# Optimization experiments

Measured on AMD Instinct MI355X. Metric: run time of the kernel, lower is better.

Reference implementation:

```python
import jax, jax.numpy as jnp
import numpy as np

N, E, DIN, D, FE, L, B, M = 10000, 40000, 11, 64, 4, 4, 512, 3


def setup_inputs() -> dict:
    key = jax.random.key(0)
    ks = iter(jax.random.split(key, 24))
    s = lambda *sh: jax.random.normal(next(ks), sh, jnp.float32)
    return {
        "x": s(N, DIN),
        "edge_index": jax.random.randint(next(ks), (2, E), 0, N),
        "edge_attr": jax.random.uniform(next(ks), (E, FE), jnp.float32),
        "batch": jnp.sort(jax.random.randint(next(ks), (N,), 0, B)),
        "W0": s(DIN, D) * 0.1, "b0": jnp.zeros((D,), jnp.float32),
        "Wn1": s(FE, 2 * D) * 0.1, "bn1": jnp.zeros((2 * D,), jnp.float32),
        "Wn2": s(2 * D, D * D) * 0.02, "bn2": jnp.zeros((D * D,), jnp.float32),
        "root": s(L, D, D) * 0.1, "conv_bias": jnp.zeros((L, D), jnp.float32),
        "lstm_Wih": s(4 * D, 2 * D) * 0.1, "lstm_Whh": s(4 * D, D) * 0.1,
        "lstm_b": jnp.zeros((4 * D,), jnp.float32),
        "Wo1": s(2 * D, D) * 0.1, "bo1": jnp.zeros((D,), jnp.float32),
        "Wo2": s(D, 1) * 0.1, "bo2": jnp.zeros((1,), jnp.float32),
    }


def reference(x, edge_index, edge_attr, batch, W0, b0, Wn1, bn1, Wn2, bn2,
              root, conv_bias, lstm_Wih, lstm_Whh, lstm_b, Wo1, bo1, Wo2, bo2):
    src, dst = edge_index[0], edge_index[1]
    h = x @ W0 + b0  # [N, D]
    # Edge MLP is SHARED across all conv layers -> compute per-edge weight matrices once
    ew = (jax.nn.silu(edge_attr @ Wn1 + bn1) @ Wn2 + bn2).reshape(E, D, D)
    for l in range(L):
        msg = jnp.einsum('ed,edf->ef', h[src], ew)  # gather-compute per edge
        aggr = jax.ops.segment_sum(msg, dst, num_segments=N)  # scatter-add to targets
        h = h + (aggr + h @ root[l] + conv_bias[l])  # NNConv + residual
    # Set2Set pooling (LSTM, M processing steps)
    q_star = jnp.zeros((B, 2 * D), h.dtype)
    hs = jnp.zeros((B, D), h.dtype)
    cs = jnp.zeros((B, D), h.dtype)
    for _ in range(M):
        gates = q_star @ lstm_Wih.T + hs @ lstm_Whh.T + lstm_b
        i, f, g, o = jnp.split(gates, 4, axis=-1)  # torch LSTM gate order
        cs = jax.nn.sigmoid(f) * cs + jax.nn.sigmoid(i) * jnp.tanh(g)
        hs = jax.nn.sigmoid(o) * jnp.tanh(cs)
        q = hs  # [B, D]
        e = jnp.sum(h * q[batch], axis=-1)  # [N]
        emax = jax.ops.segment_max(e, batch, num_segments=B)
        ex = jnp.exp(e - emax[batch])
        denom = jax.ops.segment_sum(ex, batch, num_segments=B)
        a = ex / denom[batch]  # per-graph softmax attention
        r = jax.ops.segment_sum(a[:, None] * h, batch, num_segments=B)
        q_star = jnp.concatenate([q, r], axis=-1)
    out = jax.nn.silu(q_star @ Wo1 + bo1) @ Wo2 + bo2
    return out.reshape(-1)
```

## Files before the change

### kernel.cpp

```cpp
#include <hip/hip_runtime.h>
#include <cstdint>
#include <cstddef>

#define NN   10000
#define EE   40000
#define DIN_ 11
#define DD   64
#define LL   4
#define BB   512
#define MM   3
#define K1   128
#define DD2  4096
#define NPB  16
#define CSPL 2
#define CPB  4
#define ESLOT 12
#define ECREG (8 * ESLOT)
#define GSTR 512

typedef unsigned short ushort_t;
typedef unsigned int   uint_t;

typedef __bf16 bf16x8_t __attribute__((ext_vector_type(8)));
typedef float  f32x4_t  __attribute__((ext_vector_type(4)));
union FragU { uint4 u; bf16x8_t b; };

__device__ __forceinline__ float bfu(ushort_t u) { return __uint_as_float(((uint_t)u) << 16); }
__device__ __forceinline__ float bflo(uint_t u) { return __uint_as_float(u << 16); }
__device__ __forceinline__ float bfhi(uint_t u) { return __uint_as_float(u & 0xffff0000u); }
__device__ __forceinline__ ushort_t f2bf(float f) {
  uint_t u = __float_as_uint(f);
  u = (u + 0x7fffu + ((u >> 16) & 1u)) >> 16;
  return (ushort_t)u;
}
__device__ __forceinline__ uint_t pack2(float lo, float hi) {
  return (uint_t)f2bf(lo) | ((uint_t)f2bf(hi) << 16);
}
__device__ __forceinline__ float sigmf_(float x) { return 1.f / (1.f + expf(-x)); }
__device__ __forceinline__ float siluf_(float x) { return x / (1.f + expf(-x)); }

#if defined(__HIP_DEVICE_COMPILE__) && __has_builtin(__builtin_amdgcn_fdot2_f32_bf16)
typedef __bf16 bf16x2_t __attribute__((ext_vector_type(2)));
__device__ __forceinline__ float dot2a(uint_t a, uint_t b, float c) {
  union { uint_t u; bf16x2_t v; } ua, ub;
  ua.u = a; ub.u = b;
  return __builtin_amdgcn_fdot2_f32_bf16(ua.v, ub.v, c, false);
}
#else
__device__ __forceinline__ float dot2a(uint_t a, uint_t b, float c) {
  return c + bflo(a) * bflo(b) + bfhi(a) * bfhi(b);
}
#endif

__device__ __forceinline__ int detect_bf16(const void* ea) {
  const int lane = threadIdx.x & 63;
  uint_t v = ((const uint_t*)ea)[lane];
  ushort_t a = (ushort_t)(v & 0xffffu), b = (ushort_t)(v >> 16);
  bool bad = (a & 0x8000u) || a > 0x3F80u || (b & 0x8000u) || b > 0x3F80u;
  return __ballot(bad) == 0ull ? 1 : 0;
}
__device__ __forceinline__ float ldf(const void* p, size_t i, int isbf) {
  return isbf ? bfu(((const ushort_t*)p)[i]) : ((const float*)p)[i];
}

#define PB_EMB0 256
#define PB_HIST0 (PB_EMB0 + NN / 4)
#define PB_CAN0 (PB_HIST0 + (EE + 255) / 256)
#define PB_TOTAL (PB_CAN0 + 81)
__global__ __launch_bounds__(256) void k_prep(
    const void* __restrict__ ea, const void* __restrict__ Wn2, uint_t* __restrict__ wn2m,
    const void* __restrict__ Wih, const void* __restrict__ Whh,
    float* __restrict__ Wiht, float* __restrict__ Whht,
    const void* __restrict__ x, const void* __restrict__ W0, const void* __restrict__ b0,
    const void* __restrict__ bn2, float* __restrict__ h, uint_t* __restrict__ hpk,
    float* __restrict__ nbias,
    const int* __restrict__ ei, int* __restrict__ cnt_s,
    const void* __restrict__ root, const void* __restrict__ cb,
    float* __restrict__ rootc, float* __restrict__ bn2c, float* __restrict__ cbc) {
  __shared__ ushort_t row[DD2];
  __shared__ float xs4[4][DIN_];
  __shared__ float hl4[4][DD];
  const int bx = blockIdx.x, tid = threadIdx.x;
  const int isbf = detect_bf16(ea);

  if (bx < 128) {
    const int k = bx;
    if (isbf) {
      const uint4* src = (const uint4*)((const ushort_t*)Wn2 + (size_t)k * DD2);
      ((uint4*)row)[tid] = src[tid];
      ((uint4*)row)[tid + 256] = src[tid + 256];
    } else {
      const float* src = (const float*)Wn2 + (size_t)k * DD2;
      for (int j = 0; j < 16; ++j) row[tid + 256 * j] = f2bf(src[tid + 256 * j]);
    }
    __syncthreads();
    const int kpg = k >> 1, par = k & 1;
    const int lane = tid >> 2, jp = tid & 3;
    const int q = lane >> 4, n = lane & 15;
    for (int fc = 0; fc < 4; ++fc) {
#pragma unroll
      for (int hf = 0; hf < 2; ++hf) {
        int d0 = hf * 32 + q * 8 + 2 * jp;
        int f = fc * 16 + n;
        uint_t lo = row[d0 * 64 + f], hi = row[(d0 + 1) * 64 + f];
        wn2m[((((size_t)kpg * 4 + fc) * 2 + par) * 2 + hf) * 256 + tid] = lo | (hi << 16);
      }
    }
  } else if (bx < PB_EMB0) {
    int idx = (bx - 128) * 256 + tid;
    {
      int j = idx >> 7, i = idx & 127;
      Wiht[i * 256 + j] = ldf(Wih, idx, isbf);
    }
    if (idx < 4 * DD * DD) {
      int j = idx >> 6, i = idx & 63;
      Whht[i * 256 + j] = ldf(Whh, idx, isbf);
    }
  } else if (bx < PB_HIST0) {
    const int w = tid >> 6, f = tid & 63;
    const int n = (bx - PB_EMB0) * 4 + w;
    if (f < DIN_) xs4[w][f] = ldf(x, (size_t)n * DIN_ + f, isbf);
    __syncthreads();
    float a = ldf(b0, f, isbf);
    for (int i = 0; i < DIN_; ++i) a += xs4[w][i] * ldf(W0, i * DD + f, isbf);
    h[(size_t)n * DD + f] = a;
    hl4[w][f] = a;
    float other = __shfl_down(a, 1);
    if ((f & 1) == 0)
      hpk[(size_t)n * 32 + (f >> 1)] = pack2(a, other);
    __syncthreads();
    float nb = 0.f;
#pragma unroll
    for (int d = 0; d < DD; ++d) nb += hl4[w][d] * ldf(bn2, d * DD + f, isbf);
    nbias[(size_t)n * DD + f] = nb;
  } else if (bx < PB_CAN0) {
    int e = (bx - PB_HIST0) * 256 + tid;
    if (e < EE) atomicAdd(&cnt_s[ei[e]], 1);
  } else {
    int idx = (bx - PB_CAN0) * 256 + tid;
    if (idx < LL * DD2) rootc[idx] = ldf(root, idx, isbf);
    else if (idx < LL * DD2 + DD2) bn2c[idx - LL * DD2] = ldf(bn2, idx - LL * DD2, isbf);
    else if (idx < LL * DD2 + DD2 + LL * DD)
      cbc[idx - LL * DD2 - DD2] = ldf(cb, idx - LL * DD2 - DD2, isbf);
  }
}

__global__ void k_scan(const int* __restrict__ cnt, int* __restrict__ rp,
                       const int* __restrict__ batch, int* __restrict__ goff) {
  if (blockIdx.x == 1) {
    int g = threadIdx.x;
    if (g > BB) return;
    int lo = 0, hi = NN;
    while (lo < hi) {
      int mid = (lo + hi) >> 1;
      if (batch[mid] < g) lo = mid + 1; else hi = mid;
    }
    goff[g] = lo;
    return;
  }
  __shared__ int part[1024];
  const int tid = threadIdx.x;
  const int chunk = (NN + 1023) / 1024;
  int s = 0;
  for (int j = 0; j < chunk; ++j) {
    int idx = tid * chunk + j;
    if (idx < NN) s += cnt[idx];
  }
  part[tid] = s;
  __syncthreads();
  for (int off = 1; off < 1024; off <<= 1) {
    int v = (tid >= off) ? part[tid - off] : 0;
    __syncthreads();
    part[tid] += v;
    __syncthreads();
  }
  int base = (tid == 0) ? 0 : part[tid - 1];
  for (int j = 0; j < chunk; ++j) {
    int idx = tid * chunk + j;
    if (idx < NN) { rp[idx] = base; base += cnt[idx]; }
  }
  if (tid == 1023) rp[NN] = part[1023];
}

__global__ void k_fill(const int* __restrict__ ei, const int* __restrict__ rps,
                       int* __restrict__ cur_s, int* __restrict__ epos,
                       int* __restrict__ esd) {
  int e = blockIdx.x * 256 + threadIdx.x;
  if (e >= EE) return;
  int s = ei[e], d = ei[EE + e];
  int ps = atomicAdd(&cur_s[s], 1);
  int pos = rps[s] + ps;
  epos[e] = pos;
  esd[2 * pos] = s;
  esd[2 * pos + 1] = d;
}

__global__ void k_edgemlp(const void* __restrict__ ea, const void* __restrict__ Wn1,
                          const void* __restrict__ bn1, const int* __restrict__ epos,
                          uint_t* __restrict__ hn1c) {
  const int isbf = detect_bf16(ea);
  int idx = blockIdx.x * 256 + threadIdx.x;
  if (idx >= EE * (K1 / 2)) return;
  int e = idx >> 6, j = idx & 63;
  int k0 = 2 * j, k1 = 2 * j + 1;
  float a0 = ldf(ea, e * 4 + 0, isbf), a1 = ldf(ea, e * 4 + 1, isbf);
  float a2 = ldf(ea, e * 4 + 2, isbf), a3 = ldf(ea, e * 4 + 3, isbf);
  float t0 = ldf(bn1, k0, isbf) + a0 * ldf(Wn1, k0, isbf) + a1 * ldf(Wn1, K1 + k0, isbf)
           + a2 * ldf(Wn1, 2 * K1 + k0, isbf) + a3 * ldf(Wn1, 3 * K1 + k0, isbf);
  float t1 = ldf(bn1, k1, isbf) + a0 * ldf(Wn1, k1, isbf) + a1 * ldf(Wn1, K1 + k1, isbf)
           + a2 * ldf(Wn1, 2 * K1 + k1, isbf) + a3 * ldf(Wn1, 3 * K1 + k1, isbf);
  int pos = epos[e];
  hn1c[((size_t)(j >> 3) * EE + pos) * 8 + (j & 7)] = pack2(siluf_(t0), siluf_(t1));
}

__global__ __launch_bounds__(512, 4) void k_conv(
    const uint_t* __restrict__ hpk, const uint_t* __restrict__ hn1c,
    const uint_t* __restrict__ Wn2m, const float* __restrict__ nbias,
    const int* __restrict__ rps, const int* __restrict__ esd,
    float* __restrict__ aggr) {
  __shared__ uint_t Gp[NPB * GSTR];
  __shared__ int2 eStage[ECREG];
  const int tid = threadIdx.x;
  const int w = tid >> 6, lane = tid & 63;
  const int q = lane >> 4, n16 = lane & 15;
  const int half = blockIdx.x / 625;
  const int ng = blockIdx.x - half * 625;
  const int n0 = ng * NPB;
  const int e0 = rps[n0], e1 = rps[n0 + NPB];
  const int ecnt = e1 - e0;

  if (tid < ECREG && tid < ecnt) eStage[tid] = ((const int2*)esd)[e0 + tid];

  FragU a0, a1;
  {
    const uint4* ap = (const uint4*)(hpk + (size_t)(n0 + n16) * 32);
    a0.u = ap[q];
    a1.u = ap[4 + q];
  }
  __syncthreads();

  float acc[ESLOT];
#pragma unroll
  for (int s = 0; s < ESLOT; ++s) {
    const int li = w * ESLOT + s;
    float v = 0.f;
    if (half == 0 && li < ecnt)
      v = nbias[(size_t)eStage[li].x * 64 + lane];
    acc[s] = v;
  }

  const int p = w & 3, fh = w >> 2;
  const int wkq = p >> 1, slot2 = (p & 1) * 2;
  for (int cc = 0; cc < CPB; ++cc) {
    const int c = half * CPB + cc;
    if (cc) __syncthreads();
#pragma unroll
    for (int fi = 0; fi < 2; ++fi) {
      const int fc = fh * 2 + fi;
      uint_t pk[2][4];
#pragma unroll
      for (int kk = 0; kk < 2; ++kk) {
        const int kpg = c * 8 + 2 * p + kk;
        const uint4* bp = (const uint4*)Wn2m + (size_t)(kpg * 4 + fc) * 256 + lane;
        FragU b00, b01, b10, b11;
        b00.u = bp[0];
        b01.u = bp[64];
        b10.u = bp[128];
        b11.u = bp[192];
        f32x4_t acc0 = {0.f, 0.f, 0.f, 0.f};
        f32x4_t acc1 = {0.f, 0.f, 0.f, 0.f};
        acc0 = __builtin_amdgcn_mfma_f32_16x16x32_bf16(a0.b, b00.b, acc0, 0, 0, 0);
        acc0 = __builtin_amdgcn_mfma_f32_16x16x32_bf16(a1.b, b01.b, acc0, 0, 0, 0);
        acc1 = __builtin_amdgcn_mfma_f32_16x16x32_bf16(a0.b, b10.b, acc1, 0, 0, 0);
        acc1 = __builtin_amdgcn_mfma_f32_16x16x32_bf16(a1.b, b11.b, acc1, 0, 0, 0);
#pragma unroll
        for (int r = 0; r < 4; ++r)
          pk[kk][r] = pack2(acc0[r], acc1[r]);
      }
#pragma unroll
      for (int r = 0; r < 4; ++r) {
        const int m = q * 4 + r;
        uint2 v; v.x = pk[0][r]; v.y = pk[1][r];
        *(uint2*)&Gp[(size_t)m * GSTR + (wkq * 64 + fc * 16 + n16) * 4 + slot2] = v;
      }
    }
    __syncthreads();
    int prev_src = -1;
    uint4 g0, g1;
#pragma unroll
    for (int s = 0; s < ESLOT; ++s) {
      const int li = w * ESLOT + s;
      if (li < ecnt) {
        const int2 sd = eStage[li];
        if (sd.x != prev_src) {
          prev_src = sd.x;
          const uint4* gb = (const uint4*)Gp + (size_t)(prev_src - n0) * (GSTR / 4) + lane;
          g0 = gb[0];
          g1 = gb[64];
        }
        const uint4* hp = (const uint4*)(hn1c + ((size_t)c * EE + e0 + li) * 8);
        uint4 hv0 = hp[0], hv1 = hp[1];
        float pt = acc[s];
        pt = dot2a(g0.x, hv0.x, pt);
        pt = dot2a(g0.y, hv0.y, pt);
        pt = dot2a(g0.z, hv0.z, pt);
        pt = dot2a(g0.w, hv0.w, pt);
        pt = dot2a(g1.x, hv1.x, pt);
        pt = dot2a(g1.y, hv1.y, pt);
        pt = dot2a(g1.z, hv1.z, pt);
        pt = dot2a(g1.w, hv1.w, pt);
        acc[s] = pt;
      }
    }
    for (int li = ECREG + w; li < ecnt; li += 8) {
      const int ii = e0 + li;
      const int src = __builtin_amdgcn_readfirstlane(esd[2 * ii]);
      const int dst = __builtin_amdgcn_readfirstlane(esd[2 * ii + 1]);
      const int m = src - n0;
      float pt = (half == 0 && cc == 0) ? nbias[(size_t)src * 64 + lane] : 0.f;
      const uint4* hp = (const uint4*)(hn1c + ((size_t)c * EE + ii) * 8);
      uint4 hv0 = hp[0], hv1 = hp[1];
      const uint4* gb = (const uint4*)Gp + (size_t)m * (GSTR / 4) + lane;
      uint4 og0 = gb[0], og1 = gb[64];
      pt = dot2a(og0.x, hv0.x, pt);
      pt = dot2a(og0.y, hv0.y, pt);
      pt = dot2a(og0.z, hv0.z, pt);
      pt = dot2a(og0.w, hv0.w, pt);
      pt = dot2a(og1.x, hv1.x, pt);
      pt = dot2a(og1.y, hv1.y, pt);
      pt = dot2a(og1.z, hv1.z, pt);
      pt = dot2a(og1.w, hv1.w, pt);
      atomicAdd(&aggr[(size_t)dst * 64 + lane], pt);
    }
  }
#pragma unroll
  for (int s = 0; s < ESLOT; ++s) {
    const int li = w * ESLOT + s;
    if (li < ecnt) {
      const int dst = eStage[li].y;
      atomicAdd(&aggr[(size_t)dst * 64 + lane], acc[s]);
    }
  }
}

__global__ __launch_bounds__(256) void k_update(
    float* __restrict__ h, uint_t* __restrict__ hpk,
    float* __restrict__ aggr, const float* __restrict__ bn2,
    const float* __restrict__ root, const float* __restrict__ cb,
    float* __restrict__ nbias, int l) {
  __shared__ float hl[4][DD];
  __shared__ float al[4][DD];
  const int tid = threadIdx.x, w = tid >> 6, f = tid & 63;
  const int n = blockIdx.x * 4 + w;
  float hv = h[(size_t)n * DD + f];
  hl[w][f] = hv;
  float acc = hv + aggr[(size_t)n * DD + f] + cb[l * DD + f];
  aggr[(size_t)n * DD + f] = 0.f;
  __syncthreads();
  const float* rp = root + (size_t)l * DD2;
#pragma unroll
  for (int d = 0; d < DD; ++d) acc += hl[w][d] * rp[d * DD + f];
  h[(size_t)n * DD + f] = acc;
  al[w][f] = acc;
  float other = __shfl_down(acc, 1);
  if ((f & 1) == 0)
    hpk[(size_t)n * 32 + (f >> 1)] = pack2(acc, other);
  __syncthreads();
  float nb = 0.f;
#pragma unroll
  for (int d = 0; d < DD; ++d) nb += al[w][d] * bn2[d * DD + f];
  nbias[(size_t)n * DD + f] = nb;
}

#define EVCAP 512
__global__ void k_s2s(const void* __restrict__ ea,
                      const float* __restrict__ h, const int* __restrict__ goff,
                      const float* __restrict__ Wiht, const float* __restrict__ Whht,
                      const void* __restrict__ lb,
                      const void* __restrict__ Wo1, const void* __restrict__ bo1,
                      const void* __restrict__ Wo2, const void* __restrict__ bo2,
                      void* __restrict__ outv) {
  __shared__ float qsl[K1];
  __shared__ float hsl[DD];
  __shared__ float csl[DD];
  __shared__ float gl[4][DD];
  __shared__ float red[256];
  __shared__ float ev[EVCAP];
  __shared__ float rp4[4][DD];
  const int isbf = detect_bf16(ea);
  const int g = blockIdx.x, tid = threadIdx.x;

  if (tid < K1) qsl[tid] = 0.f;
  else if (tid < K1 + DD) hsl[tid - K1] = 0.f;
  else csl[tid - K1 - DD] = 0.f;
  __syncthreads();

  const int i0 = goff[g];
  int cnt = goff[g + 1] - i0;
  if (cnt > EVCAP) cnt = EVCAP;

  for (int m = 0; m < MM; ++m) {
    {
      float a = ldf(lb, tid, isbf);
      for (int i = 0; i < K1; ++i) a += qsl[i] * Wiht[i * 256 + tid];
      for (int i = 0; i < DD; ++i) a += hsl[i] * Whht[i * 256 + tid];
      gl[tid >> 6][tid & 63] = a;
    }
    __syncthreads();
    if (tid < DD) {
      float ig = sigmf_(gl[0][tid]), fg = sigmf_(gl[1][tid]);
      float gg = tanhf(gl[2][tid]), og = sigmf_(gl[3][tid]);
      float c = fg * csl[tid] + ig * gg;
      csl[tid] = c;
      hsl[tid] = og * tanhf(c);
    }
    __syncthreads();
    float lmax = -1e30f;
    for (int jj = tid; jj < cnt; jj += 256) {
      const float* hp = h + (size_t)(i0 + jj) * DD;
      float e = 0.f;
#pragma unroll
      for (int d = 0; d < DD; ++d) e += hp[d] * hsl[d];
      ev[jj] = e;
      lmax = fmaxf(lmax, e);
    }
    red[tid] = lmax;
    __syncthreads();
    for (int s = 128; s > 0; s >>= 1) {
      if (tid < s) red[tid] = fmaxf(red[tid], red[tid + s]);
      __syncthreads();
    }
    const float emax = red[0];
    __syncthreads();
    float lsum = 0.f;
    for (int jj = tid; jj < cnt; jj += 256) {
      float ex = expf(ev[jj] - emax);
      ev[jj] = ex;
      lsum += ex;
    }
    red[tid] = lsum;
    __syncthreads();
    for (int s = 128; s > 0; s >>= 1) {
      if (tid < s) red[tid] += red[tid + s];
      __syncthreads();
    }
    const float denom = red[0];
    const int f = tid & 63, grp = tid >> 6;
    float acc = 0.f;
    for (int jj = grp; jj < cnt; jj += 4)
      acc += ev[jj] * h[(size_t)(i0 + jj) * DD + f];
    rp4[grp][f] = acc;
    __syncthreads();
    if (tid < DD) {
      float r = rp4[0][tid] + rp4[1][tid] + rp4[2][tid] + rp4[3][tid];
      r = (cnt > 0 && denom > 0.f) ? r / denom : 0.f;
      qsl[tid] = hsl[tid];
      qsl[DD + tid] = r;
    }
    __syncthreads();
  }
  if (tid < DD) {
    float t = ldf(bo1, tid, isbf);
    for (int i = 0; i < K1; ++i) t += qsl[i] * ldf(Wo1, i * DD + tid, isbf);
    float s = siluf_(t) * ldf(Wo2, tid, isbf);
    for (int off = 32; off > 0; off >>= 1) s += __shfl_down(s, off);
    if (tid == 0) {
      float v = s + ldf(bo2, 0, isbf);
      if (isbf) ((ushort_t*)outv)[g] = f2bf(v);
      else      ((float*)outv)[g] = v;
    }
  }
}

extern "C" void kernel_launch(void* const* d_in, const int* in_sizes, int n_in,
                              void* d_out, int out_size, void* d_ws, size_t ws_size,
                              hipStream_t stream) {
  const void* x_r    = d_in[0];
  const int*  ei     = (const int*)d_in[1];
  const void* ea_r   = d_in[2];
  const int*  batch  = (const int*)d_in[3];
  const void* W0_r   = d_in[4];
  const void* b0_r   = d_in[5];
  const void* Wn1_r  = d_in[6];
  const void* bn1_r  = d_in[7];
  const void* Wn2_r  = d_in[8];
  const void* bn2_r  = d_in[9];
  const void* root_r = d_in[10];
  const void* cb_r   = d_in[11];
  const void* Wih_r  = d_in[12];
  const void* Whh_r  = d_in[13];
  const void* lb_r   = d_in[14];
  const void* Wo1_r  = d_in[15];
  const void* bo1_r  = d_in[16];
  const void* Wo2_r  = d_in[17];
  const void* bo2_r  = d_in[18];

  char* w = (char*)d_ws;
  size_t off = 0;
  auto alloc = [&](size_t bytes) -> void* {
    void* p = w + off;
    off = (off + bytes + 255) & ~(size_t)255;
    return p;
  };
  float* Wiht  = (float*)alloc((size_t)K1 * 256 * 4);
  float* Whht  = (float*)alloc((size_t)DD * 256 * 4);
  float* rootc = (float*)alloc((size_t)LL * DD2 * 4);
  float* bn2c  = (float*)alloc((size_t)DD2 * 4);
  float* cbc   = (float*)alloc((size_t)LL * DD * 4);
  uint_t* Wn2m = (uint_t*)alloc((size_t)64 * 4 * 2 * 2 * 64 * 4 * 4);
  float*  h    = (float*)alloc((size_t)NN * DD * 4);
  uint_t* hpk  = (uint_t*)alloc((size_t)NN * 32 * 4);
  uint_t* hn1c = (uint_t*)alloc((size_t)EE * (K1 / 2) * 4);
  float*  aggr = (float*)alloc((size_t)NN * DD * 4);
  float*  nbias= (float*)alloc((size_t)NN * DD * 4);
  int* cnts  = (int*)alloc((size_t)2 * NN * 4);
  int* rps   = (int*)alloc((size_t)(NN + 1) * 4);
  int* epos  = (int*)alloc((size_t)EE * 4);
  int* esd   = (int*)alloc((size_t)2 * EE * 4);
  int* goff  = (int*)alloc((size_t)(BB + 1) * 4);

  int* cnt_s = cnts;
  int* cur_s = cnts + NN;

  hipMemsetAsync(cnts, 0, (size_t)2 * NN * 4, stream);
  hipMemsetAsync(aggr, 0, (size_t)NN * DD * 4, stream);

  k_prep<<<PB_TOTAL, 256, 0, stream>>>(
      ea_r, Wn2_r, Wn2m, Wih_r, Whh_r, Wiht, Whht,
      x_r, W0_r, b0_r, bn2_r, h, hpk, nbias, ei, cnt_s,
      root_r, cb_r, rootc, bn2c, cbc);
  k_scan<<<2, 1024, 0, stream>>>(cnt_s, rps, batch, goff);
  k_fill<<<(EE + 255) / 256, 256, 0, stream>>>(ei, rps, cur_s, epos, esd);
  k_edgemlp<<<(EE * (K1 / 2) + 255) / 256, 256, 0, stream>>>(ea_r, Wn1_r, bn1_r, epos, hn1c);

  for (int l = 0; l < LL; ++l) {
    k_conv<<<CSPL * (NN / NPB), 512, 0, stream>>>(hpk, hn1c, Wn2m, nbias, rps, esd, aggr);
    k_update<<<NN / 4, 256, 0, stream>>>(h, hpk, aggr, bn2c, rootc, cbc, nbias, l);
  }

  k_s2s<<<BB, 256, 0, stream>>>(ea_r, h, goff, Wiht, Whht, lb_r, Wo1_r, bo1_r, Wo2_r,
                                bo2_r, d_out);
}
```

Before: 493.6 us.

## Fuse node update into next conv layer with triple-buffered aggregates

The per-layer k_update kernel is removed. Each conv launch now recomputes the previous layer's residual update, the bf16 packing of h and the per-node bias projection into shared memory for its own 16-node tile. Aggregation buffers rotate through three arrays, so zeroing the next buffer happens inside the conv instead of in a separate pass, and a final small kernel applies the last update. Small weights are also converted once into a canonical fp32 buffer. This saves three launches and the hpk/nbias global round trips. In exchange, both CSPL halves redundantly compute the 64x64 root and bn2 matmuls for the same nodes, which adds shared memory and compute per block.

```diff
diff --git a/kernel.cpp b/kernel.cpp
--- a/kernel.cpp
+++ b/kernel.cpp
@@ -63,23 +63,36 @@
   return isbf ? bfu(((const ushort_t*)p)[i]) : ((const float*)p)[i];
 }
 
+#define CO_ROOT 0
+#define CO_BN2  16384
+#define CO_CB   20480
+#define CO_WN1  20736
+#define CO_BN1  21248
+#define CO_LB   21376
+#define CO_WO1  21632
+#define CO_BO1  29824
+#define CO_WO2  29888
+#define CO_BO2  29952
+#define CO_TOT  29953
+
 #define PB_EMB0 256
 #define PB_HIST0 (PB_EMB0 + NN / 4)
 #define PB_CAN0 (PB_HIST0 + (EE + 255) / 256)
-#define PB_TOTAL (PB_CAN0 + 81)
+#define PB_TOTAL (PB_CAN0 + (CO_TOT + 255) / 256)
 __global__ __launch_bounds__(256) void k_prep(
     const void* __restrict__ ea, const void* __restrict__ Wn2, uint_t* __restrict__ wn2m,
     const void* __restrict__ Wih, const void* __restrict__ Whh,
     float* __restrict__ Wiht, float* __restrict__ Whht,
     const void* __restrict__ x, const void* __restrict__ W0, const void* __restrict__ b0,
-    const void* __restrict__ bn2, float* __restrict__ h, uint_t* __restrict__ hpk,
-    float* __restrict__ nbias,
+    float* __restrict__ h,
     const int* __restrict__ ei, int* __restrict__ cnt_s,
-    const void* __restrict__ root, const void* __restrict__ cb,
-    float* __restrict__ rootc, float* __restrict__ bn2c, float* __restrict__ cbc) {
+    const void* __restrict__ root, const void* __restrict__ bn2, const void* __restrict__ cb,
+    const void* __restrict__ Wn1, const void* __restrict__ bn1,
+    const void* __restrict__ lb, const void* __restrict__ Wo1, const void* __restrict__ bo1,
+    const void* __restrict__ Wo2, const void* __restrict__ bo2,
+    float* __restrict__ canonbuf) {
   __shared__ ushort_t row[DD2];
   __shared__ float xs4[4][DIN_];
-  __shared__ float hl4[4][DD];
   const int bx = blockIdx.x, tid = threadIdx.x;
   const int isbf = detect_bf16(ea);
 
@@ -124,24 +137,24 @@
     float a = ldf(b0, f, isbf);
     for (int i = 0; i < DIN_; ++i) a += xs4[w][i] * ldf(W0, i * DD + f, isbf);
     h[(size_t)n * DD + f] = a;
-    hl4[w][f] = a;
-    float other = __shfl_down(a, 1);
-    if ((f & 1) == 0)
-      hpk[(size_t)n * 32 + (f >> 1)] = pack2(a, other);
-    __syncthreads();
-    float nb = 0.f;
-#pragma unroll
-    for (int d = 0; d < DD; ++d) nb += hl4[w][d] * ldf(bn2, d * DD + f, isbf);
-    nbias[(size_t)n * DD + f] = nb;
   } else if (bx < PB_CAN0) {
     int e = (bx - PB_HIST0) * 256 + tid;
     if (e < EE) atomicAdd(&cnt_s[ei[e]], 1);
   } else {
     int idx = (bx - PB_CAN0) * 256 + tid;
-    if (idx < LL * DD2) rootc[idx] = ldf(root, idx, isbf);
-    else if (idx < LL * DD2 + DD2) bn2c[idx - LL * DD2] = ldf(bn2, idx - LL * DD2, isbf);
-    else if (idx < LL * DD2 + DD2 + LL * DD)
-      cbc[idx - LL * DD2 - DD2] = ldf(cb, idx - LL * DD2 - DD2, isbf);
+    const void* src; int base;
+    if      (idx < CO_BN2) { src = root; base = CO_ROOT; }
+    else if (idx < CO_CB)  { src = bn2;  base = CO_BN2; }
+    else if (idx < CO_WN1) { src = cb;   base = CO_CB; }
+    else if (idx < CO_BN1) { src = Wn1;  base = CO_WN1; }
+    else if (idx < CO_LB)  { src = bn1;  base = CO_BN1; }
+    else if (idx < CO_WO1) { src = lb;   base = CO_LB; }
+    else if (idx < CO_BO1) { src = Wo1;  base = CO_WO1; }
+    else if (idx < CO_WO2) { src = bo1;  base = CO_BO1; }
+    else if (idx < CO_BO2) { src = Wo2;  base = CO_WO2; }
+    else if (idx < CO_TOT) { src = bo2;  base = CO_BO2; }
+    else return;
+    canonbuf[idx] = ldf(src, idx - base, isbf);
   }
 }
 
@@ -195,8 +208,8 @@
   esd[2 * pos + 1] = d;
 }
 
-__global__ void k_edgemlp(const void* __restrict__ ea, const void* __restrict__ Wn1,
-                          const void* __restrict__ bn1, const int* __restrict__ epos,
+__global__ void k_edgemlp(const void* __restrict__ ea, const float* __restrict__ Wn1,
+                          const float* __restrict__ bn1, const int* __restrict__ epos,
                           uint_t* __restrict__ hn1c) {
   const int isbf = detect_bf16(ea);
   int idx = blockIdx.x * 256 + threadIdx.x;
@@ -205,21 +218,23 @@
   int k0 = 2 * j, k1 = 2 * j + 1;
   float a0 = ldf(ea, e * 4 + 0, isbf), a1 = ldf(ea, e * 4 + 1, isbf);
   float a2 = ldf(ea, e * 4 + 2, isbf), a3 = ldf(ea, e * 4 + 3, isbf);
-  float t0 = ldf(bn1, k0, isbf) + a0 * ldf(Wn1, k0, isbf) + a1 * ldf(Wn1, K1 + k0, isbf)
-           + a2 * ldf(Wn1, 2 * K1 + k0, isbf) + a3 * ldf(Wn1, 3 * K1 + k0, isbf);
-  float t1 = ldf(bn1, k1, isbf) + a0 * ldf(Wn1, k1, isbf) + a1 * ldf(Wn1, K1 + k1, isbf)
-           + a2 * ldf(Wn1, 2 * K1 + k1, isbf) + a3 * ldf(Wn1, 3 * K1 + k1, isbf);
+  float t0 = bn1[k0] + a0 * Wn1[k0] + a1 * Wn1[K1 + k0] + a2 * Wn1[2 * K1 + k0] + a3 * Wn1[3 * K1 + k0];
+  float t1 = bn1[k1] + a0 * Wn1[k1] + a1 * Wn1[K1 + k1] + a2 * Wn1[2 * K1 + k1] + a3 * Wn1[3 * K1 + k1];
   int pos = epos[e];
   hn1c[((size_t)(j >> 3) * EE + pos) * 8 + (j & 7)] = pack2(siluf_(t0), siluf_(t1));
 }
 
 __global__ __launch_bounds__(512, 4) void k_conv(
-    const uint_t* __restrict__ hpk, const uint_t* __restrict__ hn1c,
-    const uint_t* __restrict__ Wn2m, const float* __restrict__ nbias,
+    const float* __restrict__ hR, float* __restrict__ hW,
+    const float* __restrict__ Ar, float* __restrict__ Aw, float* __restrict__ Az,
+    const uint_t* __restrict__ hn1c, const uint_t* __restrict__ Wn2m,
     const int* __restrict__ rps, const int* __restrict__ esd,
-    float* __restrict__ aggr) {
+    const float* __restrict__ rootL, const float* __restrict__ cbL,
+    const float* __restrict__ bn2c, int dofuse) {
   __shared__ uint_t Gp[NPB * GSTR];
   __shared__ int2 eStage[ECREG];
+  __shared__ float nbiasL[NPB * DD];
+  float* hscr = (float*)Gp;
   const int tid = threadIdx.x;
   const int w = tid >> 6, lane = tid & 63;
   const int q = lane >> 4, n16 = lane & 15;
@@ -230,12 +245,51 @@
   const int ecnt = e1 - e0;
 
   if (tid < ECREG && tid < ecnt) eStage[tid] = ((const int2*)esd)[e0 + tid];
-
+  for (int i = tid; i < NPB * DD; i += 512) hscr[i] = hR[(size_t)n0 * DD + i];
+  __syncthreads();
+
+  int hlb = 0;
+  if (dofuse) {
+#pragma unroll
+    for (int half2 = 0; half2 < 2; ++half2) {
+      const int idx = tid + half2 * 512;
+      const int n = idx >> 6, f = idx & 63;
+      float v = hscr[idx] + Ar[(size_t)n0 * DD + idx] + cbL[f];
+      const float* hp = hscr + n * DD;
+#pragma unroll
+      for (int d = 0; d < DD; ++d) v += hp[d] * rootL[d * DD + f];
+      hscr[1024 + idx] = v;
+      hW[(size_t)n0 * DD + idx] = v;
+      Az[(size_t)n0 * DD + idx] = 0.f;
+    }
+    hlb = 1024;
+  } else {
+#pragma unroll
+    for (int half2 = 0; half2 < 2; ++half2)
+      Az[(size_t)n0 * DD + tid + half2 * 512] = 0.f;
+  }
+  __syncthreads();
+#pragma unroll
+  for (int half2 = 0; half2 < 2; ++half2) {
+    const int idx = tid + half2 * 512;
+    const int n = idx >> 6, f = idx & 63;
+    float nb = 0.f;
+    const float* hp = hscr + hlb + n * DD;
+#pragma unroll
+    for (int d = 0; d < DD; ++d) nb += hp[d] * bn2c[d * DD + f];
+    nbiasL[idx] = nb;
+  }
   FragU a0, a1;
   {
-    const uint4* ap = (const uint4*)(hpk + (size_t)(n0 + n16) * 32);
-    a0.u = ap[q];
-    a1.u = ap[4 + q];
+    const float* hp = hscr + hlb + n16 * DD;
+    uint_t u0[4], u1[4];
+#pragma unroll
+    for (int t = 0; t < 4; ++t) {
+      u0[t] = pack2(hp[8 * q + 2 * t], hp[8 * q + 2 * t + 1]);
+      u1[t] = pack2(hp[32 + 8 * q + 2 * t], hp[32 + 8 * q + 2 * t + 1]);
+    }
+    a0.u.x = u0[0]; a0.u.y = u0[1]; a0.u.z = u0[2]; a0.u.w = u0[3];
+    a1.u.x = u1[0]; a1.u.y = u1[1]; a1.u.z = u1[2]; a1.u.w = u1[3];
   }
   __syncthreads();
 
@@ -245,7 +299,7 @@
     const int li = w * ESLOT + s;
     float v = 0.f;
     if (half == 0 && li < ecnt)
-      v = nbias[(size_t)eStage[li].x * 64 + lane];
+      v = nbiasL[(eStage[li].x - n0) * DD + lane];
     acc[s] = v;
   }
 
@@ -317,7 +371,7 @@
       const int src = __builtin_amdgcn_readfirstlane(esd[2 * ii]);
       const int dst = __builtin_amdgcn_readfirstlane(esd[2 * ii + 1]);
       const int m = src - n0;
-      float pt = (half == 0 && cc == 0) ? nbias[(size_t)src * 64 + lane] : 0.f;
+      float pt = (half == 0 && cc == 0) ? nbiasL[m * DD + lane] : 0.f;
       const uint4* hp = (const uint4*)(hn1c + ((size_t)c * EE + ii) * 8);
       uint4 hv0 = hp[0], hv1 = hp[1];
       const uint4* gb = (const uint4*)Gp + (size_t)m * (GSTR / 4) + lane;
@@ -330,7 +384,7 @@
       pt = dot2a(og1.y, hv1.y, pt);
       pt = dot2a(og1.z, hv1.z, pt);
       pt = dot2a(og1.w, hv1.w, pt);
-      atomicAdd(&aggr[(size_t)dst * 64 + lane], pt);
+      atomicAdd(&Aw[(size_t)dst * DD + lane], pt);
     }
   }
 #pragma unroll
@@ -338,47 +392,34 @@
     const int li = w * ESLOT + s;
     if (li < ecnt) {
       const int dst = eStage[li].y;
-      atomicAdd(&aggr[(size_t)dst * 64 + lane], acc[s]);
-    }
-  }
-}
-
-__global__ __launch_bounds__(256) void k_update(
-    float* __restrict__ h, uint_t* __restrict__ hpk,
-    float* __restrict__ aggr, const float* __restrict__ bn2,
-    const float* __restrict__ root, const float* __restrict__ cb,
-    float* __restrict__ nbias, int l) {
+      atomicAdd(&Aw[(size_t)dst * DD + lane], acc[s]);
+    }
+  }
+}
+
+__global__ __launch_bounds__(256) void k_upfin(
+    const float* __restrict__ hIn, const float* __restrict__ A,
+    const float* __restrict__ rootL, const float* __restrict__ cbL,
+    float* __restrict__ hOut) {
   __shared__ float hl[4][DD];
-  __shared__ float al[4][DD];
   const int tid = threadIdx.x, w = tid >> 6, f = tid & 63;
   const int n = blockIdx.x * 4 + w;
-  float hv = h[(size_t)n * DD + f];
+  float hv = hIn[(size_t)n * DD + f];
   hl[w][f] = hv;
-  float acc = hv + aggr[(size_t)n * DD + f] + cb[l * DD + f];
-  aggr[(size_t)n * DD + f] = 0.f;
+  float acc = hv + A[(size_t)n * DD + f] + cbL[f];
   __syncthreads();
-  const float* rp = root + (size_t)l * DD2;
-#pragma unroll
-  for (int d = 0; d < DD; ++d) acc += hl[w][d] * rp[d * DD + f];
-  h[(size_t)n * DD + f] = acc;
-  al[w][f] = acc;
-  float other = __shfl_down(acc, 1);
-  if ((f & 1) == 0)
-    hpk[(size_t)n * 32 + (f >> 1)] = pack2(acc, other);
-  __syncthreads();
-  float nb = 0.f;
-#pragma unroll
-  for (int d = 0; d < DD; ++d) nb += al[w][d] * bn2[d * DD + f];
-  nbias[(size_t)n * DD + f] = nb;
+#pragma unroll
+  for (int d = 0; d < DD; ++d) acc += hl[w][d] * rootL[d * DD + f];
+  hOut[(size_t)n * DD + f] = acc;
 }
 
 #define EVCAP 512
 __global__ void k_s2s(const void* __restrict__ ea,
                       const float* __restrict__ h, const int* __restrict__ goff,
                       const float* __restrict__ Wiht, const float* __restrict__ Whht,
-                      const void* __restrict__ lb,
-                      const void* __restrict__ Wo1, const void* __restrict__ bo1,
-                      const void* __restrict__ Wo2, const void* __restrict__ bo2,
+                      const float* __restrict__ lb,
+                      const float* __restrict__ Wo1, const float* __restrict__ bo1,
+                      const float* __restrict__ Wo2, const float* __restrict__ bo2,
                       void* __restrict__ outv) {
   __shared__ float qsl[K1];
   __shared__ float hsl[DD];
@@ -401,7 +442,7 @@
 
   for (int m = 0; m < MM; ++m) {
     {
-      float a = ldf(lb, tid, isbf);
+      float a = lb[tid];
       for (int i = 0; i < K1; ++i) a += qsl[i] * Wiht[i * 256 + tid];
       for (int i = 0; i < DD; ++i) a += hsl[i] * Whht[i * 256 + tid];
       gl[tid >> 6][tid & 63] = a;
@@ -460,12 +501,12 @@
     __syncthreads();
   }
   if (tid < DD) {
-    float t = ldf(bo1, tid, isbf);
-    for (int i = 0; i < K1; ++i) t += qsl[i] * ldf(Wo1, i * DD + tid, isbf);
-    float s = siluf_(t) * ldf(Wo2, tid, isbf);
+    float t = bo1[tid];
+    for (int i = 0; i < K1; ++i) t += qsl[i] * Wo1[i * DD + tid];
+    float s = siluf_(t) * Wo2[tid];
     for (int off = 32; off > 0; off >>= 1) s += __shfl_down(s, off);
     if (tid == 0) {
-      float v = s + ldf(bo2, 0, isbf);
+      float v = s + bo2[0];
       if (isbf) ((ushort_t*)outv)[g] = f2bf(v);
       else      ((float*)outv)[g] = v;
     }
@@ -504,15 +545,14 @@
   };
   float* Wiht  = (float*)alloc((size_t)K1 * 256 * 4);
   float* Whht  = (float*)alloc((size_t)DD * 256 * 4);
-  float* rootc = (float*)alloc((size_t)LL * DD2 * 4);
-  float* bn2c  = (float*)alloc((size_t)DD2 * 4);
-  float* cbc   = (float*)alloc((size_t)LL * DD * 4);
+  float* canon = (float*)alloc((size_t)CO_TOT * 4);
   uint_t* Wn2m = (uint_t*)alloc((size_t)64 * 4 * 2 * 2 * 64 * 4 * 4);
-  float*  h    = (float*)alloc((size_t)NN * DD * 4);
-  uint_t* hpk  = (uint_t*)alloc((size_t)NN * 32 * 4);
+  float*  hb0  = (float*)alloc((size_t)NN * DD * 4);
+  float*  hb1  = (float*)alloc((size_t)NN * DD * 4);
   uint_t* hn1c = (uint_t*)alloc((size_t)EE * (K1 / 2) * 4);
-  float*  aggr = (float*)alloc((size_t)NN * DD * 4);
-  float*  nbias= (float*)alloc((size_t)NN * DD * 4);
+  float*  A0   = (float*)alloc((size_t)NN * DD * 4);
+  float*  A1   = (float*)alloc((size_t)NN * DD * 4);
+  float*  A2   = (float*)alloc((size_t)NN * DD * 4);
   int* cnts  = (int*)alloc((size_t)2 * NN * 4);
   int* rps   = (int*)alloc((size_t)(NN + 1) * 4);
   int* epos  = (int*)alloc((size_t)EE * 4);
@@ -522,22 +562,38 @@
   int* cnt_s = cnts;
   int* cur_s = cnts + NN;
 
+  float* rootc = canon + CO_ROOT;
+  float* bn2c  = canon + CO_BN2;
+  float* cbc   = canon + CO_CB;
+  float* Wn1c  = canon + CO_WN1;
+  float* bn1c  = canon + CO_BN1;
+  float* lbc   = canon + CO_LB;
+  float* Wo1c  = canon + CO_WO1;
+  float* bo1c  = canon + CO_BO1;
+  float* Wo2c  = canon + CO_WO2;
+  float* bo2c  = canon + CO_BO2;
+
   hipMemsetAsync(cnts, 0, (size_t)2 * NN * 4, stream);
-  hipMemsetAsync(aggr, 0, (size_t)NN * DD * 4, stream);
+  hipMemsetAsync(A0, 0, (size_t)3 * NN * DD * 4, stream);
 
   k_prep<<<PB_TOTAL, 256, 0, stream>>>(
       ea_r, Wn2_r, Wn2m, Wih_r, Whh_r, Wiht, Whht,
-      x_r, W0_r, b0_r, bn2_r, h, hpk, nbias, ei, cnt_s,
-      root_r, cb_r, rootc, bn2c, cbc);
+      x_r, W0_r, b0_r, hb0, ei, cnt_s,
+      root_r, bn2_r, cb_r, Wn1_r, bn1_r, lb_r, Wo1_r, bo1_r, Wo2_r, bo2_r, canon);
   k_scan<<<2, 1024, 0, stream>>>(cnt_s, rps, batch, goff);
   k_fill<<<(EE + 255) / 256, 256, 0, stream>>>(ei, rps, cur_s, epos, esd);
-  k_edgemlp<<<(EE * (K1 / 2) + 255) / 256, 256, 0, stream>>>(ea_r, Wn1_r, bn1_r, epos, hn1c);
-
-  for (int l = 0; l < LL; ++l) {
-    k_conv<<<CSPL * (NN / NPB), 512, 0, stream>>>(hpk, hn1c, Wn2m, nbias, rps, esd, aggr);
-    k_update<<<NN / 4, 256, 0, stream>>>(h, hpk, aggr, bn2c, rootc, cbc, nbias, l);
-  }
-
-  k_s2s<<<BB, 256, 0, stream>>>(ea_r, h, goff, Wiht, Whht, lb_r, Wo1_r, bo1_r, Wo2_r,
-                                bo2_r, d_out);
-}
+  k_edgemlp<<<(EE * (K1 / 2) + 255) / 256, 256, 0, stream>>>(ea_r, Wn1c, bn1c, epos, hn1c);
+
+  k_conv<<<CSPL * (NN / NPB), 512, 0, stream>>>(hb0, hb1, A0, A0, A1, hn1c, Wn2m,
+                                                rps, esd, rootc, cbc, bn2c, 0);
+  k_conv<<<CSPL * (NN / NPB), 512, 0, stream>>>(hb0, hb1, A0, A1, A2, hn1c, Wn2m,
+                                                rps, esd, rootc, cbc, bn2c, 1);
+  k_conv<<<CSPL * (NN / NPB), 512, 0, stream>>>(hb1, hb0, A1, A2, A0, hn1c, Wn2m,
+                                                rps, esd, rootc + DD2, cbc + DD, bn2c, 1);
+  k_conv<<<CSPL * (NN / NPB), 512, 0, stream>>>(hb0, hb1, A2, A0, A1, hn1c, Wn2m,
+                                                rps, esd, rootc + 2 * DD2, cbc + 2 * DD, bn2c, 1);
+  k_upfin<<<NN / 4, 256, 0, stream>>>(hb1, A0, rootc + 3 * DD2, cbc + 3 * DD, hb0);
+
+  k_s2s<<<BB, 256, 0, stream>>>(ea_r, hb0, goff, Wiht, Whht, lbc, Wo1c, bo1c, Wo2c,
+                                bo2c, d_out);
+}
```

After: 706.4 us. 43.1% more time.
